# Kernel optimization log

Measured on AMD Instinct MI355X. Metric: run time of the kernel, lower is better.

The kernel has to match this reference:

```python
import jax, jax.numpy as jnp
import numpy as np

B, CIN, H, W = 256, 1280, 7, 7
A, NCLS, HID, NGT = 9, 20, 128, 40
OUT_DIM = 5 * A + NCLS  # 65


def setup_inputs() -> dict:
    key = jax.random.key(0)
    ks = jax.random.split(key, 8)
    features = jax.random.normal(ks[0], (B, CIN, H, W), jnp.float32)
    # grid: (x, y) centers of each feature cell, in feature-map coordinates
    grid = jax.random.uniform(ks[1], (B, H, W, 2), jnp.float32) * 7.0
    # GT boxes (x1, y1, x2, y2, class), padded count NGT per image
    xy1 = jax.random.uniform(ks[2], (B, NGT, 2), jnp.float32) * 5.0
    wh = jax.random.uniform(ks[3], (B, NGT, 2), jnp.float32) * 2.0 + 0.5
    cls = jax.random.randint(ks[4], (B, NGT, 1), 0, NCLS).astype(jnp.float32)
    bboxes = jnp.concatenate([xy1, xy1 + wh, cls], axis=-1)
    # anchor shapes (w, h) as in SingleStageDetector.__init__
    anc = jnp.array([[1.0, 1], [2, 2], [3, 3], [4, 4], [5, 5],
                     [2, 3], [3, 2], [3, 5], [5, 3]], jnp.float32)
    W1 = jax.random.normal(ks[5], (HID, CIN), jnp.float32) * 0.02
    b1 = jnp.zeros((HID,), jnp.float32)
    W2 = jax.random.normal(ks[6], (OUT_DIM, HID), jnp.float32) * 0.02
    b2 = jnp.zeros((OUT_DIM,), jnp.float32)
    return dict(features=features, grid=grid, bboxes=bboxes, anc=anc,
                W1=W1, b1=b1, W2=W2, b2=b2)


def reference(features, grid, bboxes, anc, W1, b1, W2, b2):
    Bx = features.shape[0]
    # --- PredictionNetwork (inference mode; dropout is identity at eval) ---
    h = jnp.einsum('bchw,oc->bohw', features, W1) + b1[None, :, None, None]
    h = jax.nn.leaky_relu(h, negative_slope=0.01)
    out = jnp.einsum('bchw,oc->bohw', h, W2) + b2[None, :, None, None]
    conf_scores = jax.nn.sigmoid(out[:, 4 * A:5 * A])          # (B, A, H, W)
    offsets = out[:, :4 * A].reshape(Bx, A, 4, H, W)
    offsets = jnp.concatenate(
        [jax.nn.sigmoid(offsets[:, :, :2]) - 0.5, offsets[:, :, 2:]], axis=2)
    class_scores = out[:, 5 * A:]                               # (B, C, H, W)
    # --- GenerateAnchor: (B, A, H, W, 4) as (x_tl, y_tl, x_br, y_br) ---
    ctr = grid[:, None]                    # (B, 1, H, W, 2)
    half = anc[None, :, None, None, :] / 2  # (1, A, 1, 1, 2)
    anchors = jnp.concatenate([ctr - half, ctr + half], axis=-1)
    # --- IoU: (B, A*H*W, N) ---
    P = anchors.reshape(Bx, -1, 4)          # (B, AHW, 4)
    gt = bboxes[..., :4]                    # (B, N, 4)
    tl = jnp.maximum(P[:, :, None, :2], gt[:, None, :, :2])
    br = jnp.minimum(P[:, :, None, 2:], gt[:, None, :, 2:])
    inter = jnp.prod(jnp.clip(br - tl, 0.0), axis=-1)  # (B, AHW, N)
    # torch code zeroes intersections for proposals with any coord <= 0
    legal = (jnp.min(P, axis=-1) > 0)[..., None]
    inter = inter * legal
    p_area = ((P[:, :, 2] - P[:, :, 0]) * (P[:, :, 3] - P[:, :, 1]))[:, :, None]
    g_area = ((gt[:, :, 2] - gt[:, :, 0]) * (gt[:, :, 3] - gt[:, :, 1]))[:, None, :]
    iou_mat = inter / (g_area + p_area - inter)
    return (conf_scores, offsets, class_scores, iou_mat)
```

## Files before the change

kernel.cpp:

```cpp
#include <hip/hip_runtime.h>


#define CIN_  1280
#define HW_   49
#define HID_  128
#define OUTD_ 65
#define NGT_  40
#define NP_   441

#define CONF_OFF 0
#define OFFS_OFF 112896
#define CLS_OFF  564480
#define IOU_OFF  815360

#define WS_W1F_U32 81920u
#define WS_W2F_U32 5120u

typedef __bf16 bf16x8 __attribute__((ext_vector_type(8)));
typedef float  f32x4  __attribute__((ext_vector_type(4)));

__device__ __forceinline__ unsigned pack2bf(float lo, float hi) {
    unsigned a = __float_as_uint(lo);
    unsigned b = __float_as_uint(hi);
    a = (a + 0x7FFFu + ((a >> 16) & 1u)) >> 16;
    b = (b + 0x7FFFu + ((b >> 16) & 1u)) >> 16;
    return a | (b << 16);
}
__device__ __forceinline__ float sigmoidf_(float v) { return 1.f / (1.f + __expf(-v)); }

__device__ __forceinline__ bf16x8 ld_frag(const unsigned* p) {
    union { uint4 u; bf16x8 v; } x;
    x.u = *(const uint4*)p;
    return x.v;
}
__device__ __forceinline__ bf16x8 as_bf(uint4 u) {
    union { uint4 u; bf16x8 v; } x; x.u = u; return x.v;
}

__global__ __launch_bounds__(256) void prep_w(
    const float* __restrict__ W1, const float* __restrict__ W2,
    unsigned* __restrict__ ws)
{
    int X = blockIdx.x * 256 + threadIdx.x;
    if (X < (int)WS_W1F_U32) {
        int sub = X & 3, lane = (X >> 2) & 63, f = X >> 8;
        int mt = f & 7, K32 = f >> 3;
        int o = mt * 16 + (lane & 15);
        int c = K32 * 32 + (lane >> 4) * 8 + sub * 2;
        float2 v = *(const float2*)(W1 + o * CIN_ + c);
        ws[X] = pack2bf(v.x, v.y);
    } else {
        int Y = X - (int)WS_W1F_U32;
        int sub = Y & 3, lane = (Y >> 2) & 63, f = Y >> 8;
        int mt2 = f % 5, ks2 = f / 5;
        int o2 = mt2 * 16 + (lane & 15);
        int c = ks2 * 32 + (lane >> 4) * 8 + sub * 2;
        unsigned val = 0;
        if (o2 < OUTD_) {
            float2 v = *(const float2*)(W2 + o2 * HID_ + c);
            val = pack2bf(v.x, v.y);
        }
        ws[WS_W1F_U32 + Y] = val;
    }
}

__global__ __launch_bounds__(512, 4) void fused_main(
    const float* __restrict__ F,
    const float* __restrict__ grd,
    const float* __restrict__ bbox,
    const float* __restrict__ anc,
    const unsigned* __restrict__ wsW,
    const float* __restrict__ B1,
    const float* __restrict__ B2,
    float* __restrict__ out)
{
    __shared__ __align__(16) unsigned lds[32 * 640];
    unsigned* smHT = lds;

    const int tid  = threadIdx.x;
    const int b    = blockIdx.x >> 1;
    const int half = blockIdx.x & 1;
    const int lane = tid & 63;
    const int w    = tid >> 6;
    const int quad = lane >> 4;
    const int m16  = lane & 15;
    const int hw0  = half * 32;

    const float* Fb = F + b * (CIN_ * HW_);

    #pragma unroll
    for (int g = 0; g < 5; ++g) {
        float f0[8], f1[8];
        #pragma unroll
        for (int u = 0; u < 8; ++u) {
            int i   = (g * 8 + u) * 512 + tid;
            int cp  = i >> 5;
            int row = i & 31;
            int hw  = hw0 + row;
            bool ok = hw < HW_;
            f0[u] = ok ? Fb[(2 * cp) * HW_ + hw] : 0.f;
            f1[u] = ok ? Fb[(2 * cp + 1) * HW_ + hw] : 0.f;
        }
        #pragma unroll
        for (int u = 0; u < 8; ++u) {
            int i   = (g * 8 + u) * 512 + tid;
            int cp  = i >> 5;
            int row = i & 31;
            int cb = cp >> 2, sub = cp & 3;
            lds[row * 640 + ((cb ^ (row & 7)) << 2) + sub] = pack2bf(f0[u], f1[u]);
        }
    }
    __syncthreads();

    const uint4* Ap = (const uint4*)wsW + w * 64 + lane;
    const unsigned* r0b = lds + m16 * 640;
    const unsigned* r1b = lds + (16 + m16) * 640;
    const int swz = (m16 & 7);

    f32x4 acc0 = (f32x4)(0.f), acc1 = (f32x4)(0.f);
    uint4 a0 = Ap[0];
    uint4 a1 = Ap[512];
    for (int k = 0; k < 40; ++k) {
        uint4 an;
        if (k < 38) an = Ap[(k + 2) * 512];
        int off = ((k * 4 + quad) ^ swz) << 2;
        bf16x8 A = as_bf(a0);
        bf16x8 b0 = ld_frag(r0b + off);
        bf16x8 b1 = ld_frag(r1b + off);
        acc0 = __builtin_amdgcn_mfma_f32_16x16x32_bf16(A, b0, acc0, 0, 0, 0);
        acc1 = __builtin_amdgcn_mfma_f32_16x16x32_bf16(A, b1, acc1, 0, 0, 0);
        a0 = a1; a1 = an;
    }

    const int m2a = w % 5, nt2a = w / 5;
    const uint4* A2p = (const uint4*)(wsW + WS_W1F_U32) + m2a * 64 + lane;
    uint4 a20 = A2p[0], a21 = A2p[320], a22 = A2p[640], a23 = A2p[960];

    __syncthreads();

    #pragma unroll
    for (int nt = 0; nt < 2; ++nt) {
        f32x4 ac = nt ? acc1 : acc0;
        int r0 = nt * 16 + m16;
        #pragma unroll
        for (int rp = 0; rp < 2; ++rp) {
            int o0 = w * 16 + quad * 4 + 2 * rp;
            float v0 = ac[2 * rp]     + B1[o0];
            float v1 = ac[2 * rp + 1] + B1[o0 + 1];
            v0 = v0 > 0.f ? v0 : 0.01f * v0;
            v1 = v1 > 0.f ? v1 : 0.01f * v1;
            smHT[r0 * 68 + (o0 >> 1)] = pack2bf(v0, v1);
        }
    }
    __syncthreads();

    {
        f32x4 c2 = (f32x4)(0.f);
        const unsigned* Bb = smHT + (nt2a * 16 + m16) * 68 + quad * 4;
        c2 = __builtin_amdgcn_mfma_f32_16x16x32_bf16(as_bf(a20), ld_frag(Bb +  0), c2, 0, 0, 0);
        c2 = __builtin_amdgcn_mfma_f32_16x16x32_bf16(as_bf(a21), ld_frag(Bb + 16), c2, 0, 0, 0);
        c2 = __builtin_amdgcn_mfma_f32_16x16x32_bf16(as_bf(a22), ld_frag(Bb + 32), c2, 0, 0, 0);
        c2 = __builtin_amdgcn_mfma_f32_16x16x32_bf16(as_bf(a23), ld_frag(Bb + 48), c2, 0, 0, 0);
        int hw = hw0 + nt2a * 16 + m16;
        if (hw < HW_) {
            #pragma unroll
            for (int r = 0; r < 4; ++r) {
                int o2 = m2a * 16 + quad * 4 + r;
                if (o2 >= OUTD_) continue;
                float aa = c2[r] + B2[o2];
                unsigned dst; float val;
                if (o2 < 36) {
                    int an9 = o2 >> 2, kk = o2 & 3;
                    val = (kk < 2) ? (sigmoidf_(aa) - 0.5f) : aa;
                    dst = OFFS_OFF + b * 1764 + an9 * 196 + kk * 49 + hw;
                } else if (o2 < 45) {
                    val = sigmoidf_(aa);
                    dst = CONF_OFF + b * 441 + (o2 - 36) * 49 + hw;
                } else {
                    val = aa;
                    dst = CLS_OFF + b * 980 + (o2 - 45) * 49 + hw;
                }
                out[dst] = val;
            }
        }
    }
    if (w < 2) {
        const int m2b = 3 + w;
        const uint4* A3p = (const uint4*)(wsW + WS_W1F_U32) + m2b * 64 + lane;
        uint4 b20 = A3p[0], b21 = A3p[320], b22 = A3p[640], b23 = A3p[960];
        f32x4 c2 = (f32x4)(0.f);
        const unsigned* Bb = smHT + (16 + m16) * 68 + quad * 4;
        c2 = __builtin_amdgcn_mfma_f32_16x16x32_bf16(as_bf(b20), ld_frag(Bb +  0), c2, 0, 0, 0);
        c2 = __builtin_amdgcn_mfma_f32_16x16x32_bf16(as_bf(b21), ld_frag(Bb + 16), c2, 0, 0, 0);
        c2 = __builtin_amdgcn_mfma_f32_16x16x32_bf16(as_bf(b22), ld_frag(Bb + 32), c2, 0, 0, 0);
        c2 = __builtin_amdgcn_mfma_f32_16x16x32_bf16(as_bf(b23), ld_frag(Bb + 48), c2, 0, 0, 0);
        int hw = hw0 + 16 + m16;
        if (hw < HW_) {
            #pragma unroll
            for (int r = 0; r < 4; ++r) {
                int o2 = m2b * 16 + quad * 4 + r;
                if (o2 >= OUTD_) continue;
                float aa = c2[r] + B2[o2];
                unsigned dst; float val;
                if (o2 < 36) {
                    int an9 = o2 >> 2, kk = o2 & 3;
                    val = (kk < 2) ? (sigmoidf_(aa) - 0.5f) : aa;
                    dst = OFFS_OFF + b * 1764 + an9 * 196 + kk * 49 + hw;
                } else if (o2 < 45) {
                    val = sigmoidf_(aa);
                    dst = CONF_OFF + b * 441 + (o2 - 36) * 49 + hw;
                } else {
                    val = aa;
                    dst = CLS_OFF + b * 980 + (o2 - 45) * 49 + hw;
                }
                out[dst] = val;
            }
        }
    }

    {
        int gl = (lane < NGT_) ? lane : 0;
        const float* gb = bbox + b * 200 + gl * 5;
        float gx1 = gb[0], gy1 = gb[1], gx2 = gb[2], gy2 = gb[3];
        float gA = (gx2 - gx1) * (gy2 - gy1);
        const int pstart = half ? 221 : 0;
        const int pend   = half ? NP_ : 221;
        #pragma unroll 4
        for (int p = pstart + w; p < pend; p += 8) {
            int a9 = p / 49, r = p - a9 * 49;
            float2 ct = *(const float2*)(grd + b * 98 + 2 * r);
            float hx = anc[2 * a9] * 0.5f,  hy = anc[2 * a9 + 1] * 0.5f;
            float px1 = ct.x - hx, py1 = ct.y - hy, px2 = ct.x + hx, py2 = ct.y + hy;
            float pA = (px2 - px1) * (py2 - py1);
            float legal = (fminf(fminf(px1, py1), fminf(px2, py2)) > 0.f) ? 1.f : 0.f;
            float tlx = fmaxf(px1, gx1), tly = fmaxf(py1, gy1);
            float brx = fminf(px2, gx2), bry = fminf(py2, gy2);
            float dx = fmaxf(brx - tlx, 0.f), dy = fmaxf(bry - tly, 0.f);
            float inter = dx * dy * legal;
            float iou = inter / (gA + pA - inter);
            if (lane < NGT_)
                out[IOU_OFF + b * (NP_ * NGT_) + p * 40 + lane] = iou;
        }
    }
}

extern "C" void kernel_launch(void* const* d_in, const int* in_sizes, int n_in,
                              void* d_out, int out_size, void* d_ws, size_t ws_size,
                              hipStream_t stream) {
    const float* F  = (const float*)d_in[0];
    const float* G  = (const float*)d_in[1];
    const float* BB = (const float*)d_in[2];
    const float* AN = (const float*)d_in[3];
    const float* W1 = (const float*)d_in[4];
    const float* B1 = (const float*)d_in[5];
    const float* W2 = (const float*)d_in[6];
    const float* B2 = (const float*)d_in[7];
    float* out = (float*)d_out;
    unsigned* wsu = (unsigned*)d_ws;

    prep_w<<<340, 256, 0, stream>>>(W1, W2, wsu);
    fused_main<<<512, 512, 0, stream>>>(F, G, BB, AN, wsu, B1, B2, out);
}
```

Baseline: 133.4 us.

## Split each image into four 16-pixel blocks to double grid size

Each block now covers 16 spatial positions instead of 32, so the grid grows from 512 to 1024 blocks. LDS use is halved and the launch-bounds occupancy hint is raised from 4 to 6. The aim is more resident blocks and better latency hiding for the feature loads. The cost is that every W1 fragment is streamed from global/L2 twice as many times per image, since each block reuses it across only one MFMA tile. The IoU work is also interleaved across the four blocks.

```diff
diff --git a/kernel.cpp b/kernel.cpp
--- a/kernel.cpp
+++ b/kernel.cpp
@@ -64,7 +64,7 @@
     }
 }
 
-__global__ __launch_bounds__(512, 4) void fused_main(
+__global__ __launch_bounds__(512, 6) void fused_main(
     const float* __restrict__ F,
     const float* __restrict__ grd,
     const float* __restrict__ bbox,
@@ -74,38 +74,38 @@
     const float* __restrict__ B2,
     float* __restrict__ out)
 {
-    __shared__ __align__(16) unsigned lds[32 * 640];
+    __shared__ __align__(16) unsigned lds[16 * 640];
     unsigned* smHT = lds;
 
     const int tid  = threadIdx.x;
-    const int b    = blockIdx.x >> 1;
-    const int half = blockIdx.x & 1;
+    const int b    = blockIdx.x >> 2;
+    const int q    = blockIdx.x & 3;
     const int lane = tid & 63;
     const int w    = tid >> 6;
     const int quad = lane >> 4;
     const int m16  = lane & 15;
-    const int hw0  = half * 32;
+    const int hw0  = q * 16;
 
     const float* Fb = F + b * (CIN_ * HW_);
 
     #pragma unroll
-    for (int g = 0; g < 5; ++g) {
-        float f0[8], f1[8];
+    for (int g = 0; g < 2; ++g) {
+        float f0[10], f1[10];
         #pragma unroll
-        for (int u = 0; u < 8; ++u) {
-            int i   = (g * 8 + u) * 512 + tid;
-            int cp  = i >> 5;
-            int row = i & 31;
+        for (int u = 0; u < 10; ++u) {
+            int i   = (g * 10 + u) * 512 + tid;
+            int cp  = i >> 4;
+            int row = i & 15;
             int hw  = hw0 + row;
             bool ok = hw < HW_;
             f0[u] = ok ? Fb[(2 * cp) * HW_ + hw] : 0.f;
             f1[u] = ok ? Fb[(2 * cp + 1) * HW_ + hw] : 0.f;
         }
         #pragma unroll
-        for (int u = 0; u < 8; ++u) {
-            int i   = (g * 8 + u) * 512 + tid;
-            int cp  = i >> 5;
-            int row = i & 31;
+        for (int u = 0; u < 10; ++u) {
+            int i   = (g * 10 + u) * 512 + tid;
+            int cp  = i >> 4;
+            int row = i & 15;
             int cb = cp >> 2, sub = cp & 3;
             lds[row * 640 + ((cb ^ (row & 7)) << 2) + sub] = pack2bf(f0[u], f1[u]);
         }
@@ -113,11 +113,10 @@
     __syncthreads();
 
     const uint4* Ap = (const uint4*)wsW + w * 64 + lane;
-    const unsigned* r0b = lds + m16 * 640;
-    const unsigned* r1b = lds + (16 + m16) * 640;
+    const unsigned* rb = lds + m16 * 640;
     const int swz = (m16 & 7);
 
-    f32x4 acc0 = (f32x4)(0.f), acc1 = (f32x4)(0.f);
+    f32x4 acc = (f32x4)(0.f);
     uint4 a0 = Ap[0];
     uint4 a1 = Ap[512];
     for (int k = 0; k < 40; ++k) {
@@ -125,47 +124,42 @@
         if (k < 38) an = Ap[(k + 2) * 512];
         int off = ((k * 4 + quad) ^ swz) << 2;
         bf16x8 A = as_bf(a0);
-        bf16x8 b0 = ld_frag(r0b + off);
-        bf16x8 b1 = ld_frag(r1b + off);
-        acc0 = __builtin_amdgcn_mfma_f32_16x16x32_bf16(A, b0, acc0, 0, 0, 0);
-        acc1 = __builtin_amdgcn_mfma_f32_16x16x32_bf16(A, b1, acc1, 0, 0, 0);
+        bf16x8 Bf = ld_frag(rb + off);
+        acc = __builtin_amdgcn_mfma_f32_16x16x32_bf16(A, Bf, acc, 0, 0, 0);
         a0 = a1; a1 = an;
     }
 
-    const int m2a = w % 5, nt2a = w / 5;
-    const uint4* A2p = (const uint4*)(wsW + WS_W1F_U32) + m2a * 64 + lane;
-    uint4 a20 = A2p[0], a21 = A2p[320], a22 = A2p[640], a23 = A2p[960];
+    uint4 a20, a21, a22, a23;
+    if (w < 5) {
+        const uint4* A2p = (const uint4*)(wsW + WS_W1F_U32) + w * 64 + lane;
+        a20 = A2p[0]; a21 = A2p[320]; a22 = A2p[640]; a23 = A2p[960];
+    }
 
     __syncthreads();
 
     #pragma unroll
-    for (int nt = 0; nt < 2; ++nt) {
-        f32x4 ac = nt ? acc1 : acc0;
-        int r0 = nt * 16 + m16;
-        #pragma unroll
-        for (int rp = 0; rp < 2; ++rp) {
-            int o0 = w * 16 + quad * 4 + 2 * rp;
-            float v0 = ac[2 * rp]     + B1[o0];
-            float v1 = ac[2 * rp + 1] + B1[o0 + 1];
-            v0 = v0 > 0.f ? v0 : 0.01f * v0;
-            v1 = v1 > 0.f ? v1 : 0.01f * v1;
-            smHT[r0 * 68 + (o0 >> 1)] = pack2bf(v0, v1);
-        }
+    for (int rp = 0; rp < 2; ++rp) {
+        int o0 = w * 16 + quad * 4 + 2 * rp;
+        float v0 = acc[2 * rp]     + B1[o0];
+        float v1 = acc[2 * rp + 1] + B1[o0 + 1];
+        v0 = v0 > 0.f ? v0 : 0.01f * v0;
+        v1 = v1 > 0.f ? v1 : 0.01f * v1;
+        smHT[m16 * 68 + (o0 >> 1)] = pack2bf(v0, v1);
     }
     __syncthreads();
 
-    {
+    if (w < 5) {
         f32x4 c2 = (f32x4)(0.f);
-        const unsigned* Bb = smHT + (nt2a * 16 + m16) * 68 + quad * 4;
+        const unsigned* Bb = smHT + m16 * 68 + quad * 4;
         c2 = __builtin_amdgcn_mfma_f32_16x16x32_bf16(as_bf(a20), ld_frag(Bb +  0), c2, 0, 0, 0);
         c2 = __builtin_amdgcn_mfma_f32_16x16x32_bf16(as_bf(a21), ld_frag(Bb + 16), c2, 0, 0, 0);
         c2 = __builtin_amdgcn_mfma_f32_16x16x32_bf16(as_bf(a22), ld_frag(Bb + 32), c2, 0, 0, 0);
         c2 = __builtin_amdgcn_mfma_f32_16x16x32_bf16(as_bf(a23), ld_frag(Bb + 48), c2, 0, 0, 0);
-        int hw = hw0 + nt2a * 16 + m16;
+        int hw = hw0 + m16;
         if (hw < HW_) {
             #pragma unroll
             for (int r = 0; r < 4; ++r) {
-                int o2 = m2a * 16 + quad * 4 + r;
+                int o2 = w * 16 + quad * 4 + r;
                 if (o2 >= OUTD_) continue;
                 float aa = c2[r] + B2[o2];
                 unsigned dst; float val;
@@ -184,49 +178,14 @@
             }
         }
     }
-    if (w < 2) {
-        const int m2b = 3 + w;
-        const uint4* A3p = (const uint4*)(wsW + WS_W1F_U32) + m2b * 64 + lane;
-        uint4 b20 = A3p[0], b21 = A3p[320], b22 = A3p[640], b23 = A3p[960];
-        f32x4 c2 = (f32x4)(0.f);
-        const unsigned* Bb = smHT + (16 + m16) * 68 + quad * 4;
-        c2 = __builtin_amdgcn_mfma_f32_16x16x32_bf16(as_bf(b20), ld_frag(Bb +  0), c2, 0, 0, 0);
-        c2 = __builtin_amdgcn_mfma_f32_16x16x32_bf16(as_bf(b21), ld_frag(Bb + 16), c2, 0, 0, 0);
-        c2 = __builtin_amdgcn_mfma_f32_16x16x32_bf16(as_bf(b22), ld_frag(Bb + 32), c2, 0, 0, 0);
-        c2 = __builtin_amdgcn_mfma_f32_16x16x32_bf16(as_bf(b23), ld_frag(Bb + 48), c2, 0, 0, 0);
-        int hw = hw0 + 16 + m16;
-        if (hw < HW_) {
-            #pragma unroll
-            for (int r = 0; r < 4; ++r) {
-                int o2 = m2b * 16 + quad * 4 + r;
-                if (o2 >= OUTD_) continue;
-                float aa = c2[r] + B2[o2];
-                unsigned dst; float val;
-                if (o2 < 36) {
-                    int an9 = o2 >> 2, kk = o2 & 3;
-                    val = (kk < 2) ? (sigmoidf_(aa) - 0.5f) : aa;
-                    dst = OFFS_OFF + b * 1764 + an9 * 196 + kk * 49 + hw;
-                } else if (o2 < 45) {
-                    val = sigmoidf_(aa);
-                    dst = CONF_OFF + b * 441 + (o2 - 36) * 49 + hw;
-                } else {
-                    val = aa;
-                    dst = CLS_OFF + b * 980 + (o2 - 45) * 49 + hw;
-                }
-                out[dst] = val;
-            }
-        }
-    }
 
     {
         int gl = (lane < NGT_) ? lane : 0;
         const float* gb = bbox + b * 200 + gl * 5;
         float gx1 = gb[0], gy1 = gb[1], gx2 = gb[2], gy2 = gb[3];
         float gA = (gx2 - gx1) * (gy2 - gy1);
-        const int pstart = half ? 221 : 0;
-        const int pend   = half ? NP_ : 221;
         #pragma unroll 4
-        for (int p = pstart + w; p < pend; p += 8) {
+        for (int p = q + 4 * w; p < NP_; p += 32) {
             int a9 = p / 49, r = p - a9 * 49;
             float2 ct = *(const float2*)(grd + b * 98 + 2 * r);
             float hx = anc[2 * a9] * 0.5f,  hy = anc[2 * a9 + 1] * 0.5f;
@@ -259,5 +218,5 @@
     unsigned* wsu = (unsigned*)d_ws;
 
     prep_w<<<340, 256, 0, stream>>>(W1, W2, wsu);
-    fused_main<<<512, 512, 0, stream>>>(F, G, BB, AN, wsu, B1, B2, out);
-}
+    fused_main<<<1024, 512, 0, stream>>>(F, G, BB, AN, wsu, B1, B2, out);
+}
```

After: 145.4 us. +9.0%, slower.
